# Kernel tuning notes

Measured on AMD Instinct MI355X. Metric: run time of the kernel, lower is better.

## Reference

```python
import jax, jax.numpy as jnp
import numpy as np

GROUPS = 32
EPS = 1e-6

def groupnorm(x, gamma, beta):
    b, c, h, w = x.shape
    xg = x.reshape(b, GROUPS, c // GROUPS, h, w)
    mu = xg.mean(axis=(2, 3, 4), keepdims=True)
    var = xg.var(axis=(2, 3, 4), keepdims=True)
    xn = ((xg - mu) / jnp.sqrt(var + EPS)).reshape(b, c, h, w)
    return xn * gamma[None, :, None, None] + beta[None, :, None, None]

def conv1x1(x, w, b):
    return jnp.einsum('oc,bchw->bohw', w, x) + b[None, :, None, None]

def attn_branch(xn, wq, bq, wk, bk, v_flat, scale):
    q = conv1x1(xn, wq, bq)
    k = conv1x1(xn, wk, bk)
    b_, c, h, w = q.shape
    qf = q.reshape(b_, c, h * w)   # b c n
    kf = k.reshape(b_, c, h * w)   # b c n
    scores = jnp.einsum('bci,bcj->bij', qf, kf) * scale  # b n n
    attn = jax.nn.softmax(scores, axis=2)
    out = jnp.einsum('bcj,bij->bci', v_flat, attn)       # b c n
    return out.reshape(b_, c, h, w)

def setup_inputs() -> dict:
    key = jax.random.key(0)
    ks = jax.random.split(key, 14)
    B, C, H, W = 4, 64, 64, 64
    R = C // 16  # SE reduction
    s = 0.05
    return {
        'x1': jax.random.normal(ks[0], (B, C, H, W), jnp.float32),
        'x2': jax.random.normal(ks[1], (B, C, H, W), jnp.float32),
        'se_w1': jax.random.normal(ks[2], (R, C), jnp.float32) * s,
        'se_w2': jax.random.normal(ks[3], (C, R), jnp.float32) * s,
        'gn_gamma': jnp.ones((C,), jnp.float32),
        'gn_beta': jnp.zeros((C,), jnp.float32),
        'wq': jax.random.normal(ks[4], (C, C), jnp.float32) * s,
        'bq': jnp.zeros((C,), jnp.float32),
        'wk': jax.random.normal(ks[5], (C, C), jnp.float32) * s,
        'bk': jnp.zeros((C,), jnp.float32),
        'wv': jax.random.normal(ks[6], (C, C), jnp.float32) * s,
        'bv': jnp.zeros((C,), jnp.float32),
    }

def reference(x1, x2, se_w1, se_w2, gn_gamma, gn_beta, wq, bq, wk, bk, wv, bv):
    x = x1 + x2
    # SE channel attention (ends in sigmoid), then an EXTRA sigmoid as in source
    y = x.mean(axis=(2, 3))                         # b c
    y = jax.nn.relu(y @ se_w1.T)                    # b r
    y = jax.nn.sigmoid(y @ se_w2.T)                 # b c
    se = x * y[:, :, None, None]
    ch_w = jax.nn.sigmoid(se)
    xn = groupnorm(x, gn_gamma, gn_beta)
    v = conv1x1(xn, wv, bv)
    b_, c, h, w = v.shape
    v_flat = v.reshape(b_, c, h * w)
    scale = 1.0 / jnp.sqrt(jnp.float32(c))
    # source reuses q1/k1 convs for BOTH branches
    h1 = attn_branch(groupnorm(x1, gn_gamma, gn_beta), wq, bq, wk, bk, v_flat, scale)
    h2 = attn_branch(groupnorm(x2, gn_gamma, gn_beta), wq, bq, wk, bk, v_flat, scale)
    return 2.0 * h1 * ch_w + 2.0 * h2 * (1.0 - ch_w)
```

## Files before the change

### kernel.cpp

```cpp
#include <hip/hip_runtime.h>

#define STATS_OFF 0
#define AD_OFF    20480
#define SEY_OFF   26624
#define BIAS_OFF  27648
#define WQB_OFF   32768
#define WKB_OFF   40960
#define WVB_OFF   49152
#define Q_OFF     57344
#define K_OFF     (Q_OFF + 4194304)
#define V_OFF     (K_OFF + 4194304)
#define PO_OFF    (V_OFF + 2097152)

#define QSCALE 0.18033688f

typedef __attribute__((ext_vector_type(8))) short  short8;
typedef __attribute__((ext_vector_type(4))) short  s16x4;
typedef __attribute__((ext_vector_type(2))) unsigned int u32x2;
typedef __attribute__((ext_vector_type(4))) float  f32x4;

#if __has_builtin(__builtin_amdgcn_mfma_f32_16x16x16bf16_1k)
#define HAS_1K 1
#else
#define HAS_1K 0
#endif

__device__ inline ushort f2b(float f) {
  return (ushort)((__float_as_uint(f) + 0x8000u) >> 16);
}
__device__ inline unsigned pack2(float x, float y) {
  unsigned ux = __float_as_uint(x) + 0x8000u;
  unsigned uy = __float_as_uint(y) + 0x8000u;
  return __builtin_amdgcn_perm(uy, ux, 0x07060302);
}
__device__ inline float b2f(ushort u) { return __uint_as_float(((unsigned)u) << 16); }

__device__ inline f32x4 mfma16(short8 a, short8 b, f32x4 c) {
  return __builtin_amdgcn_mfma_f32_16x16x32_bf16(a, b, c, 0, 0, 0);
}

__device__ inline float wsum64(float v) {
  #pragma unroll
  for (int o = 32; o > 0; o >>= 1) v += __shfl_down(v, o, 64);
  return v;
}

__global__ __launch_bounds__(256) void sc_stats(const float* __restrict__ x1,
                                                const float* __restrict__ x2,
                                                float* __restrict__ stats) {
  int blk = blockIdx.x;
  int bc = blk >> 2, chunk = blk & 3;
  const float4* p1 = (const float4*)(x1 + (size_t)bc * 4096 + chunk * 1024);
  const float4* p2 = (const float4*)(x2 + (size_t)bc * 4096 + chunk * 1024);
  float4 a = p1[threadIdx.x], b = p2[threadIdx.x];
  float s1 = a.x + a.y + a.z + a.w;
  float q1 = a.x*a.x + a.y*a.y + a.z*a.z + a.w*a.w;
  float s2 = b.x + b.y + b.z + b.w;
  float q2 = b.x*b.x + b.y*b.y + b.z*b.z + b.w*b.w;
  float p12 = a.x*b.x + a.y*b.y + a.z*b.z + a.w*b.w;
  s1 = wsum64(s1); q1 = wsum64(q1); s2 = wsum64(s2); q2 = wsum64(q2); p12 = wsum64(p12);
  __shared__ float red[4][5];
  int w = threadIdx.x >> 6, ln = threadIdx.x & 63;
  if (ln == 0) { red[w][0] = s1; red[w][1] = q1; red[w][2] = s2; red[w][3] = q2; red[w][4] = p12; }
  __syncthreads();
  if (threadIdx.x < 5) {
    float acc = 0;
    #pragma unroll
    for (int ww = 0; ww < 4; ww++) acc += red[ww][threadIdx.x];
    stats[(size_t)blk * 5 + threadIdx.x] = acc;
  }
}

__global__ __launch_bounds__(256) void sc_prep(const float* __restrict__ stats,
                                               const float* __restrict__ w1,
                                               const float* __restrict__ w2,
                                               const float* __restrict__ gamma,
                                               const float* __restrict__ beta,
                                               const float* __restrict__ wq, const float* __restrict__ bq,
                                               const float* __restrict__ wk, const float* __restrict__ bk,
                                               const float* __restrict__ wv, const float* __restrict__ bv,
                                               float* __restrict__ ad, float* __restrict__ sey,
                                               float* __restrict__ biasbuf,
                                               ushort* __restrict__ wqb, ushort* __restrict__ wkb,
                                               ushort* __restrict__ wvb) {
  int t = threadIdx.x; int b = t >> 6, c = t & 63;
  float s1 = 0, q1 = 0, s2 = 0, q2 = 0, p12 = 0;
  #pragma unroll
  for (int ch = 0; ch < 4; ch++) {
    const float* sp = stats + (size_t)(t * 4 + ch) * 5;
    s1 += sp[0]; q1 += sp[1]; s2 += sp[2]; q2 += sp[3]; p12 += sp[4];
  }
  float sx = s1 + s2, qx = q1 + q2 + 2.f * p12;
  __shared__ float smu[256], sS[3][256], sQ[3][256], sy[16], sdd[3][256];
  smu[t] = sx * (1.f / 4096.f);
  sS[0][t] = sx; sQ[0][t] = qx; sS[1][t] = s1; sQ[1][t] = q1; sS[2][t] = s2; sQ[2][t] = q2;
  __syncthreads();
  if (t < 16) {
    int bb = t >> 2, r = t & 3; float acc = 0.f;
    for (int cc = 0; cc < 64; cc++) acc += w1[r*64+cc] * smu[bb*64+cc];
    sy[t] = fmaxf(acc, 0.f);
  }
  __syncthreads();
  float acc = 0.f;
  #pragma unroll
  for (int r = 0; r < 4; r++) acc += w2[c*4+r] * sy[b*4+r];
  sey[t] = 1.f / (1.f + exp2f(-acc * 1.44269504f));
  int prt = t ^ 1;
  float g = gamma[c], bt = beta[c];
  #pragma unroll
  for (int s = 0; s < 3; s++) {
    float S = sS[s][t] + sS[s][prt], Q = sQ[s][t] + sQ[s][prt];
    float mean = S * (1.f / 8192.f);
    float var  = Q * (1.f / 8192.f) - mean * mean;
    float rstd = rsqrtf(var + 1e-6f);
    float a = g * rstd;
    float d = bt - mean * a;
    ad[((s*256) + t)*2 + 0] = a;
    ad[((s*256) + t)*2 + 1] = d;
    sdd[s][t] = d;
  }
  __syncthreads();
  #pragma unroll
  for (int k = 0; k < 5; k++) {
    int idx = k * 256 + t;
    const float* W; const float* bs; const float* dd; int o; float scale = 1.f;
    if (idx < 256)      { int bb = idx >> 6; o = idx & 63; W = wv; bs = bv; dd = &sdd[0][bb*64]; }
    else if (idx < 768) { int r = idx - 256; int bh = r >> 6; o = r & 63; W = wq; bs = bq;
                          dd = &sdd[1 + (bh & 1)][(bh >> 1)*64]; scale = QSCALE; }
    else                { int r = idx - 768; int bh = r >> 6; o = r & 63; W = wk; bs = bk;
                          dd = &sdd[1 + (bh & 1)][(bh >> 1)*64]; }
    float a2 = bs[o];
    for (int cc = 0; cc < 64; cc++) a2 += W[o*64+cc] * dd[cc];
    biasbuf[idx] = a2 * scale;
  }
  for (int i = t; i < 4096; i += 256) {
    wqb[i] = f2b(wq[i] * QSCALE);
    wkb[i] = f2b(wk[i]);
    wvb[i] = f2b(wv[i]);
  }
}

__global__ __launch_bounds__(256) void sc_proj(const float* __restrict__ x1, const float* __restrict__ x2,
    const float* __restrict__ ad, const float* __restrict__ biasbuf,
    const ushort* __restrict__ wqb, const ushort* __restrict__ wkb, const ushort* __restrict__ wvb,
    ushort* __restrict__ qout, ushort* __restrict__ kout, ushort* __restrict__ vout) {
  int pt = blockIdx.x, src = blockIdx.y, b = blockIdx.z, t = threadIdx.x;
  __shared__ ushort xlds[64 * 66];
  __shared__ float sbias[2][64];
  if (t < 128) {
    int proj = t >> 6, o = t & 63;
    float bb;
    if (src == 0) bb = (proj == 0) ? biasbuf[b*64 + o] : 0.f;
    else          bb = biasbuf[256 + (proj ? 512 : 0) + (b*2 + src - 1)*64 + o];
    sbias[proj][o] = bb;
  }
  {
    int c = t >> 2, pq = (t & 3) * 16;
    const float* px1 = x1 + ((size_t)(b*64 + c))*4096 + pt*64 + pq;
    const float* px2 = x2 + ((size_t)(b*64 + c))*4096 + pt*64 + pq;
    float av = ad[((src*256) + b*64 + c)*2 + 0];
    #pragma unroll
    for (int k4 = 0; k4 < 4; k4++) {
      float4 v1 = *(const float4*)(px1 + 4*k4);
      float xv[4];
      if (src == 1) { xv[0]=v1.x; xv[1]=v1.y; xv[2]=v1.z; xv[3]=v1.w; }
      else {
        float4 v2 = *(const float4*)(px2 + 4*k4);
        if (src == 2) { xv[0]=v2.x; xv[1]=v2.y; xv[2]=v2.z; xv[3]=v2.w; }
        else { xv[0]=v1.x+v2.x; xv[1]=v1.y+v2.y; xv[2]=v1.z+v2.z; xv[3]=v1.w+v2.w; }
      }
      #pragma unroll
      for (int k = 0; k < 4; k++)
        xlds[(pq + 4*k4 + k)*66 + c] = f2b(av * xv[k]);
    }
  }
  __syncthreads();
  int wave = t >> 6, lane = t & 63, quad = lane >> 4, l15 = lane & 15;
  if (src == 0) {
    const ushort* ap = wvb + (wave*16 + l15)*64 + quad*8;
    short8 a0 = *(const short8*)ap;
    short8 a1 = *(const short8*)(ap + 32);
    f32x4 cinit;
    #pragma unroll
    for (int r = 0; r < 4; r++) cinit[r] = sbias[0][wave*16 + quad*4 + r];
    #pragma unroll
    for (int s = 0; s < 4; s++) {
      const ushort* bp = xlds + (s*16 + l15)*66 + quad*8;
      short8 b0 = *(const short8*)bp;
      short8 b1 = *(const short8*)(bp + 32);
      f32x4 acc = mfma16(a0, b0, cinit);
      acc = mfma16(a1, b1, acc);
      #pragma unroll
      for (int r = 0; r < 4; r++)
        vout[((size_t)(b*64 + wave*16 + quad*4 + r))*4096 + pt*64 + s*16 + l15] = f2b(acc[r]);
    }
  } else {
    int bh = b*2 + (src - 1);
    const ushort* ap = xlds + (wave*16 + l15)*66 + quad*8;
    short8 a0 = *(const short8*)ap;
    short8 a1 = *(const short8*)(ap + 32);
    #pragma unroll
    for (int proj = 0; proj < 2; proj++) {
      const ushort* Wb = proj == 0 ? wqb : wkb;
      ushort* dst = proj == 0 ? qout : kout;
      #pragma unroll
      for (int s = 0; s < 4; s++) {
        const ushort* bp = Wb + (s*16 + l15)*64 + quad*8;
        short8 b0 = *(const short8*)bp;
        short8 b1 = *(const short8*)(bp + 32);
        float bb = sbias[proj][s*16 + l15];
        f32x4 acc = {bb, bb, bb, bb};
        acc = mfma16(a0, b0, acc);
        acc = mfma16(a1, b1, acc);
        #pragma unroll
        for (int r = 0; r < 4; r++)
          dst[((size_t)bh*4096 + pt*64 + wave*16 + quad*4 + r)*64 + s*16 + l15] = f2b(acc[r]);
      }
    }
  }
}

__global__ __launch_bounds__(256, 4) void sc_flash(const ushort* __restrict__ qg,
                                                   const ushort* __restrict__ kg,
                                                   const ushort* __restrict__ vg,
                                                   ushort* __restrict__ po,
                                                   float* __restrict__ pl,
                                                   int jsbits) {
  int blk = blockIdx.x;
  int bh = blk & 7, rest = blk >> 3;
  int njs = 1 << jsbits, njt = 64 >> jsbits;
  int js = rest & (njs - 1), itile = rest >> jsbits;
  int jbase = js * (njt << 6);
  int b = bh >> 1;
  int t = threadIdx.x, wave = t >> 6, lane = t & 63, quad = lane >> 4, l15 = lane & 15;
  int i0 = itile * 128 + wave * 32;

  __shared__ ushort Klds[64 * 72];
  __shared__ ushort Vlds[64 * 72];
#if !HAS_1K
  __shared__ ushort Plds[4][32 * 72];
#endif

  const ushort* qbase = qg + ((size_t)bh * 4096 + i0 + l15) * 64 + quad * 8;
  short8 Qb[2][2];
  Qb[0][0] = *(const short8*)qbase;
  Qb[0][1] = *(const short8*)(qbase + 32);
  Qb[1][0] = *(const short8*)(qbase + 16 * 64);
  Qb[1][1] = *(const short8*)(qbase + 16 * 64 + 32);

  f32x4 O[2][4]; const f32x4 zero4 = {0.f, 0.f, 0.f, 0.f};
  #pragma unroll
  for (int ib = 0; ib < 2; ib++)
    #pragma unroll
    for (int cb = 0; cb < 4; cb++) O[ib][cb] = zero4;
  float lsum[2] = {0.f, 0.f};

  int sr = t >> 2, sc = (t & 3) * 16;
  const ushort* ksrc = kg + ((size_t)bh * 4096 + jbase + sr) * 64 + sc;
  const ushort* vsrc = vg + ((size_t)(b * 64 + sr)) * 4096 + jbase + sc;
  ushort* kdst = Klds + sr * 72 + sc;
  ushort* vdst = Vlds + sr * 72 + sc;

  uint4 kr0 = *(const uint4*)ksrc, kr1 = *(const uint4*)(ksrc + 8);
  uint4 vr0 = *(const uint4*)vsrc, vr1 = *(const uint4*)(vsrc + 8);
  ksrc += 4096; vsrc += 64;

  #pragma unroll 1
  for (int jt = 0; jt < njt; jt++) {
    __syncthreads();
    *(uint4*)kdst = kr0; *(uint4*)(kdst + 8) = kr1;
    *(uint4*)vdst = vr0; *(uint4*)(vdst + 8) = vr1;
    __syncthreads();
    if (jt + 1 < njt) {
      kr0 = *(const uint4*)ksrc; kr1 = *(const uint4*)(ksrc + 8);
      vr0 = *(const uint4*)vsrc; vr1 = *(const uint4*)(vsrc + 8);
      ksrc += 4096; vsrc += 64;
    }

    f32x4 S[2][4];
    #pragma unroll
    for (int s = 0; s < 4; s++) {
      const ushort* kp = Klds + (s * 16 + l15) * 72 + quad * 8;
      short8 ka0 = *(const short8*)kp;
      short8 ka1 = *(const short8*)(kp + 32);
      #pragma unroll
      for (int ib = 0; ib < 2; ib++) {
        f32x4 acc = mfma16(ka0, Qb[ib][0], zero4);
        S[ib][s] = mfma16(ka1, Qb[ib][1], acc);
      }
    }

#if HAS_1K
    s16x4 Pb[2][4];
#endif
    #pragma unroll
    for (int ib = 0; ib < 2; ib++) {
      #pragma unroll
      for (int s = 0; s < 4; s++) {
        float p0 = exp2f(S[ib][s][0]);
        float p1 = exp2f(S[ib][s][1]);
        float p2 = exp2f(S[ib][s][2]);
        float p3 = exp2f(S[ib][s][3]);
        lsum[ib] += (p0 + p1) + (p2 + p3);
#if HAS_1K
        u32x2 wpk = {pack2(p0, p1), pack2(p2, p3)};
        Pb[ib][s] = __builtin_bit_cast(s16x4, wpk);
#else
        ushort* pw = &Plds[wave][(ib * 16 + l15) * 72 + s * 16 + quad * 4];
        pw[0] = f2b(p0); pw[1] = f2b(p1); pw[2] = f2b(p2); pw[3] = f2b(p3);
#endif
      }
    }

#if HAS_1K
    #pragma unroll
    for (int s = 0; s < 4; s++) {
      #pragma unroll
      for (int cb = 0; cb < 4; cb++) {
        s16x4 vb = *(const s16x4*)(Vlds + (cb * 16 + l15) * 72 + s * 16 + quad * 4);
        O[0][cb] = __builtin_amdgcn_mfma_f32_16x16x16bf16_1k(Pb[0][s], vb, O[0][cb], 0, 0, 0);
        O[1][cb] = __builtin_amdgcn_mfma_f32_16x16x16bf16_1k(Pb[1][s], vb, O[1][cb], 0, 0, 0);
      }
    }
#else
    __threadfence_block();
    #pragma unroll
    for (int ib = 0; ib < 2; ib++) {
      short8 pa0 = *(const short8*)&Plds[wave][(ib * 16 + l15) * 72 + quad * 8];
      short8 pa1 = *(const short8*)&Plds[wave][(ib * 16 + l15) * 72 + quad * 8 + 32];
      #pragma unroll
      for (int cb = 0; cb < 4; cb++) {
        const ushort* vbp = Vlds + (cb * 16 + l15) * 72 + quad * 8;
        short8 v0 = *(const short8*)vbp;
        short8 v1 = *(const short8*)(vbp + 32);
        O[ib][cb] = mfma16(pa0, v0, O[ib][cb]);
        O[ib][cb] = mfma16(pa1, v1, O[ib][cb]);
      }
    }
#endif
  }

  size_t slice = (size_t)(bh * njs + js) * 4096;
  #pragma unroll
  for (int ib = 0; ib < 2; ib++) {
    float lv = lsum[ib];
    lv += __shfl_xor(lv, 16, 64);
    lv += __shfl_xor(lv, 32, 64);
    if (quad == 0) pl[slice + i0 + ib * 16 + l15] = lv;
    #pragma unroll
    for (int cb = 0; cb < 4; cb++)
      #pragma unroll
      for (int r = 0; r < 4; r++)
        po[(slice + i0 + ib * 16 + quad * 4 + r) * 64 + cb * 16 + l15] = f2b(O[ib][cb][r]);
  }
}

__global__ __launch_bounds__(256) void sc_combine(const float* __restrict__ x1, const float* __restrict__ x2,
                                                  const ushort* __restrict__ po, const float* __restrict__ pl,
                                                  const float* __restrict__ sey,
                                                  float* __restrict__ out, int jsbits) {
  int njs = 1 << jsbits;
  int itile = blockIdx.x, b = blockIdx.y, ch = blockIdx.z, t = threadIdx.x;
  __shared__ float hl[2][32 * 65];
  #pragma unroll
  for (int head = 0; head < 2; head++) {
    int bh = b * 2 + head;
    int i = t >> 2, c8 = (t & 3) * 8;
    float sum[8];
    #pragma unroll
    for (int k = 0; k < 8; k++) sum[k] = 0.f;
    float lacc = 0.f;
    for (int js = 0; js < njs; js++) {
      size_t base = ((size_t)(bh * njs + js)) * 4096;
      uint4 u = *(const uint4*)(po + base * 64 + (size_t)(itile * 64 + i) * 64 + ch * 32 + c8);
      const ushort* us = (const ushort*)&u;
      #pragma unroll
      for (int k = 0; k < 8; k++) sum[k] += b2f(us[k]);
      lacc += pl[base + itile * 64 + i];
    }
    float inv = 1.f / lacc;
    #pragma unroll
    for (int k = 0; k < 8; k++) hl[head][(c8 + k) * 65 + i] = sum[k] * inv;
  }
  __syncthreads();
  #pragma unroll
  for (int it = 0; it < 8; it++) {
    int idx = it * 256 + t;
    int cl = idx >> 6, p = idx & 63;
    int c = ch * 32 + cl;
    size_t gi = ((size_t)(b * 64 + c)) * 4096 + itile * 64 + p;
    float xv = x1[gi] + x2[gi];
    float sig = 1.f / (1.f + exp2f(-xv * sey[b * 64 + c] * 1.44269504f));
    float h1 = hl[0][cl * 65 + p], h2 = hl[1][cl * 65 + p];
    out[gi] = 2.f * (h1 * sig + h2 * (1.f - sig));
  }
}

extern "C" void kernel_launch(void* const* d_in, const int* in_sizes, int n_in,
                              void* d_out, int out_size, void* d_ws, size_t ws_size,
                              hipStream_t stream) {
  (void)in_sizes; (void)n_in; (void)out_size;
  const float* x1    = (const float*)d_in[0];
  const float* x2    = (const float*)d_in[1];
  const float* se_w1 = (const float*)d_in[2];
  const float* se_w2 = (const float*)d_in[3];
  const float* gamma = (const float*)d_in[4];
  const float* beta  = (const float*)d_in[5];
  const float* wq    = (const float*)d_in[6];
  const float* bq    = (const float*)d_in[7];
  const float* wk    = (const float*)d_in[8];
  const float* bk    = (const float*)d_in[9];
  const float* wv    = (const float*)d_in[10];
  const float* bv    = (const float*)d_in[11];
  float* out = (float*)d_out;
  char* ws = (char*)d_ws;
  float*  stats = (float*)(ws + STATS_OFF);
  float*  ad    = (float*)(ws + AD_OFF);
  float*  sey   = (float*)(ws + SEY_OFF);
  float*  biasb = (float*)(ws + BIAS_OFF);
  ushort* wqb   = (ushort*)(ws + WQB_OFF);
  ushort* wkb   = (ushort*)(ws + WKB_OFF);
  ushort* wvb   = (ushort*)(ws + WVB_OFF);
  ushort* qb    = (ushort*)(ws + Q_OFF);
  ushort* kb    = (ushort*)(ws + K_OFF);
  ushort* vb    = (ushort*)(ws + V_OFF);

  size_t need4 = (size_t)PO_OFF + (size_t)8 * 4 * 4096 * 64 * 2 + (size_t)8 * 4 * 4096 * 4;
  int jsbits = (ws_size >= need4) ? 2 : 1;
  int njs = 1 << jsbits;
  ushort* pob = (ushort*)(ws + PO_OFF);
  float*  plb = (float*)(ws + PO_OFF + (size_t)8 * njs * 4096 * 64 * 2);

  sc_stats  <<<1024, 256, 0, stream>>>(x1, x2, stats);
  sc_prep   <<<1, 256, 0, stream>>>(stats, se_w1, se_w2, gamma, beta,
                                    wq, bq, wk, bk, wv, bv,
                                    ad, sey, biasb, wqb, wkb, wvb);
  sc_proj   <<<dim3(64, 3, 4), 256, 0, stream>>>(x1, x2, ad, biasb,
                                                 wqb, wkb, wvb, qb, kb, vb);
  sc_flash  <<<8 * 32 * njs, 256, 0, stream>>>(qb, kb, vb, pob, plb, jsbits);
  sc_combine<<<dim3(64, 4, 2), 256, 0, stream>>>(x1, x2, pob, plb, sey, out, jsbits);
}
```

Baseline: 175.5 us.

## Stage projection outputs in LDS, use fast exp2, raise flash occupancy and split

The projection kernel now writes its MFMA results into an LDS tile and then emits coalesced 16-byte global stores, replacing scattered 2-byte stores. exp2f calls are replaced by the hardware exp2 builtin in the flash, prep and combine kernels. The flash kernel's launch bounds ask for 8 blocks per CU instead of 4, and the key dimension can now be split into 8 chunks when the workspace is large enough. Splitting more adds partial-output traffic and reduction work in the combine step, and the tighter register budget may cause spills.

```diff
diff --git a/kernel.cpp b/kernel.cpp
--- a/kernel.cpp
+++ b/kernel.cpp
@@ -23,6 +23,12 @@
 #define HAS_1K 1
 #else
 #define HAS_1K 0
+#endif
+
+#if __has_builtin(__builtin_amdgcn_exp2f)
+__device__ inline float fexp2(float x) { return __builtin_amdgcn_exp2f(x); }
+#else
+__device__ inline float fexp2(float x) { return exp2f(x); }
 #endif
 
 __device__ inline ushort f2b(float f) {
@@ -104,7 +110,7 @@
   float acc = 0.f;
   #pragma unroll
   for (int r = 0; r < 4; r++) acc += w2[c*4+r] * sy[b*4+r];
-  sey[t] = 1.f / (1.f + exp2f(-acc * 1.44269504f));
+  sey[t] = 1.f / (1.f + fexp2(-acc * 1.44269504f));
   int prt = t ^ 1;
   float g = gamma[c], bt = beta[c];
   #pragma unroll
@@ -146,6 +152,7 @@
     ushort* __restrict__ qout, ushort* __restrict__ kout, ushort* __restrict__ vout) {
   int pt = blockIdx.x, src = blockIdx.y, b = blockIdx.z, t = threadIdx.x;
   __shared__ ushort xlds[64 * 66];
+  __shared__ ushort olds[64 * 66];
   __shared__ float sbias[2][64];
   if (t < 128) {
     int proj = t >> 6, o = t & 63;
@@ -176,6 +183,7 @@
   }
   __syncthreads();
   int wave = t >> 6, lane = t & 63, quad = lane >> 4, l15 = lane & 15;
+  int orow = t >> 2, ocol = (t & 3) * 16;
   if (src == 0) {
     const ushort* ap = wvb + (wave*16 + l15)*64 + quad*8;
     short8 a0 = *(const short8*)ap;
@@ -192,8 +200,13 @@
       acc = mfma16(a1, b1, acc);
       #pragma unroll
       for (int r = 0; r < 4; r++)
-        vout[((size_t)(b*64 + wave*16 + quad*4 + r))*4096 + pt*64 + s*16 + l15] = f2b(acc[r]);
-    }
+        olds[(wave*16 + quad*4 + r)*66 + s*16 + l15] = f2b(acc[r]);
+    }
+    __syncthreads();
+    uint4 w0 = *(const uint4*)&olds[orow*66 + ocol];
+    uint4 w1 = *(const uint4*)&olds[orow*66 + ocol + 8];
+    ushort* dst = vout + ((size_t)(b*64 + orow))*4096 + pt*64 + ocol;
+    *(uint4*)dst = w0; *(uint4*)(dst + 8) = w1;
   } else {
     int bh = b*2 + (src - 1);
     const ushort* ap = xlds + (wave*16 + l15)*66 + quad*8;
@@ -214,13 +227,19 @@
         acc = mfma16(a1, b1, acc);
         #pragma unroll
         for (int r = 0; r < 4; r++)
-          dst[((size_t)bh*4096 + pt*64 + wave*16 + quad*4 + r)*64 + s*16 + l15] = f2b(acc[r]);
-      }
-    }
-  }
-}
-
-__global__ __launch_bounds__(256, 4) void sc_flash(const ushort* __restrict__ qg,
+          olds[(wave*16 + quad*4 + r)*66 + s*16 + l15] = f2b(acc[r]);
+      }
+      __syncthreads();
+      uint4 w0 = *(const uint4*)&olds[orow*66 + ocol];
+      uint4 w1 = *(const uint4*)&olds[orow*66 + ocol + 8];
+      ushort* dp = dst + ((size_t)bh*4096 + pt*64 + orow)*64 + ocol;
+      *(uint4*)dp = w0; *(uint4*)(dp + 8) = w1;
+      if (proj == 0) __syncthreads();
+    }
+  }
+}
+
+__global__ __launch_bounds__(256, 8) void sc_flash(const ushort* __restrict__ qg,
                                                    const ushort* __restrict__ kg,
                                                    const ushort* __restrict__ vg,
                                                    ushort* __restrict__ po,
@@ -297,10 +316,10 @@
     for (int ib = 0; ib < 2; ib++) {
       #pragma unroll
       for (int s = 0; s < 4; s++) {
-        float p0 = exp2f(S[ib][s][0]);
-        float p1 = exp2f(S[ib][s][1]);
-        float p2 = exp2f(S[ib][s][2]);
-        float p3 = exp2f(S[ib][s][3]);
+        float p0 = fexp2(S[ib][s][0]);
+        float p1 = fexp2(S[ib][s][1]);
+        float p2 = fexp2(S[ib][s][2]);
+        float p3 = fexp2(S[ib][s][3]);
         lsum[ib] += (p0 + p1) + (p2 + p3);
 #if HAS_1K
         u32x2 wpk = {pack2(p0, p1), pack2(p2, p3)};
@@ -390,7 +409,7 @@
     int c = ch * 32 + cl;
     size_t gi = ((size_t)(b * 64 + c)) * 4096 + itile * 64 + p;
     float xv = x1[gi] + x2[gi];
-    float sig = 1.f / (1.f + exp2f(-xv * sey[b * 64 + c] * 1.44269504f));
+    float sig = 1.f / (1.f + fexp2(-xv * sey[b * 64 + c] * 1.44269504f));
     float h1 = hl[0][cl * 65 + p], h2 = hl[1][cl * 65 + p];
     out[gi] = 2.f * (h1 * sig + h2 * (1.f - sig));
   }
@@ -425,8 +444,11 @@
   ushort* kb    = (ushort*)(ws + K_OFF);
   ushort* vb    = (ushort*)(ws + V_OFF);
 
-  size_t need4 = (size_t)PO_OFF + (size_t)8 * 4 * 4096 * 64 * 2 + (size_t)8 * 4 * 4096 * 4;
-  int jsbits = (ws_size >= need4) ? 2 : 1;
+  int jsbits = 1;
+  for (int jb = 3; jb >= 2; jb--) {
+    size_t need = (size_t)PO_OFF + ((size_t)8 * 4096 * 64 * 2 + (size_t)8 * 4096 * 4) * (1u << jb);
+    if (ws_size >= need) { jsbits = jb; break; }
+  }
   int njs = 1 << jsbits;
   ushort* pob = (ushort*)(ws + PO_OFF);
   float*  plb = (float*)(ws + PO_OFF + (size_t)8 * njs * 4096 * 64 * 2);
```

After: 452.3 us. 2.58x slower.
